# Kernel tuning notes

Measured on AMD Instinct MI355X. Metric: run time of the kernel, lower is better.

## Reference

```python
import jax, jax.numpy as jnp
import numpy as np

NEG = -1e6

def setup_inputs() -> dict:
    key = jax.random.key(0)
    ks = jax.random.split(key, 7)
    B, Q, K, H, Dv = 16, 64, 1024, 256, 256
    return {
        "queries": jax.random.normal(ks[0], (B, Q, H), jnp.float32),
        "keys": jax.random.normal(ks[1], (B, K, H), jnp.float32),
        "values": jax.random.normal(ks[2], (B, K, Dv), jnp.float32),
        "valid_lens": jax.random.randint(ks[3], (B,), 1, K + 1),
        "Wq": jax.random.normal(ks[4], (H, H), jnp.float32) / np.sqrt(H),
        "Wk": jax.random.normal(ks[5], (H, H), jnp.float32) / np.sqrt(H),
        "wv": jax.random.normal(ks[6], (H,), jnp.float32) / np.sqrt(H),
    }

def reference(queries, keys, values, valid_lens, Wq, Wk, wv):
    # projections: [B,Q,H], [B,K,H]
    q = jnp.einsum("bqd,hd->bqh", queries, Wq)
    k = jnp.einsum("bkd,hd->bkh", keys, Wk)
    # broadcast add + tanh: [B,Q,K,H]
    features = jnp.tanh(q[:, :, None, :] + k[:, None, :, :])
    # score reduction over hidden: [B,Q,K]
    scores = jnp.einsum("bqkh,h->bqk", features, wv)
    # masked softmax over the key axis (1D valid_lens per batch)
    K = keys.shape[1]
    mask = jnp.arange(K)[None, None, :] < valid_lens[:, None, None]  # [B,1,K]
    scores = jnp.where(mask, scores, NEG)
    attn = jax.nn.softmax(scores, axis=-1)
    # weighted sum over values: [B,Q,Dv]
    return jnp.einsum("bqk,bkv->bqv", attn, values)
```

## Files before the change

kernel.cpp:

```cpp
#include <hip/hip_runtime.h>

#define LOG2E 1.4426950408889634f
#define TANH_SCALE 2.8853900817779268f
#define NEG_BIG -1e30f

typedef __attribute__((ext_vector_type(8))) short bf16x8;
typedef __attribute__((ext_vector_type(4))) float f32x4;

static __device__ __forceinline__ short f2bf(float f) {
    unsigned u = __builtin_bit_cast(unsigned, f);
    u += 0x7fffu + ((u >> 16) & 1u);
    return (short)(u >> 16);
}

__global__ __launch_bounds__(256) void proj_mfma(const float* __restrict__ queries,
                                                 const float* __restrict__ keys,
                                                 const float* __restrict__ Wq,
                                                 const float* __restrict__ Wk,
                                                 float* __restrict__ qp,
                                                 float* __restrict__ kp) {
    const int mtile = blockIdx.x;
    const float* A; const float* W; float* dst; int m0;
    if (mtile < 16) { A = queries; W = Wq; dst = qp; m0 = mtile * 64; }
    else            { A = keys;    W = Wk; dst = kp; m0 = (mtile - 16) * 64; }

    const int tid  = threadIdx.x;
    const int w    = tid >> 6;
    const int lane = tid & 63;
    const int wm   = w >> 1, wn = w & 1;
    const int row_base = m0 + wm * 32;
    const int col_base = blockIdx.y * 128 + wn * 64;
    const int r  = lane & 15;
    const int kq = lane >> 4;

    f32x4 acc[2][4] = {};

    #pragma unroll
    for (int ks = 0; ks < 8; ++ks) {
        const int k0 = ks * 32 + kq * 8;
        bf16x8 a[2], bb[4];
        #pragma unroll
        for (int mi = 0; mi < 2; ++mi) {
            const float* p = &A[(row_base + mi * 16 + r) * 256 + k0];
            float4 f0 = *reinterpret_cast<const float4*>(p);
            float4 f1 = *reinterpret_cast<const float4*>(p + 4);
            a[mi] = (bf16x8){f2bf(f0.x), f2bf(f0.y), f2bf(f0.z), f2bf(f0.w),
                             f2bf(f1.x), f2bf(f1.y), f2bf(f1.z), f2bf(f1.w)};
        }
        #pragma unroll
        for (int nj = 0; nj < 4; ++nj) {
            const float* p = &W[(col_base + nj * 16 + r) * 256 + k0];
            float4 f0 = *reinterpret_cast<const float4*>(p);
            float4 f1 = *reinterpret_cast<const float4*>(p + 4);
            bb[nj] = (bf16x8){f2bf(f0.x), f2bf(f0.y), f2bf(f0.z), f2bf(f0.w),
                              f2bf(f1.x), f2bf(f1.y), f2bf(f1.z), f2bf(f1.w)};
        }
        #pragma unroll
        for (int mi = 0; mi < 2; ++mi)
            #pragma unroll
            for (int nj = 0; nj < 4; ++nj)
                acc[mi][nj] = __builtin_amdgcn_mfma_f32_16x16x32_bf16(a[mi], bb[nj], acc[mi][nj], 0, 0, 0);
    }

    #pragma unroll
    for (int mi = 0; mi < 2; ++mi)
        #pragma unroll
        for (int nj = 0; nj < 4; ++nj)
            #pragma unroll
            for (int t = 0; t < 4; ++t)
                dst[(row_base + mi * 16 + kq * 4 + t) * 256 + col_base + nj * 16 + r] =
                    acc[mi][nj][t] * TANH_SCALE;
}

__global__ __launch_bounds__(256) void attn_kernel(const float* __restrict__ qp,
                                                   const float* __restrict__ kp,
                                                   const float* __restrict__ values,
                                                   const int* __restrict__ valid_lens,
                                                   const float* __restrict__ wv,
                                                   float* __restrict__ part_acc,
                                                   float* __restrict__ part_m,
                                                   float* __restrict__ part_l) {
    __shared__ float4 kp_t[64 * 32];
    __shared__ float4 qp_f4[4 * 64];
    __shared__ float4 wv2_f4[64];
    __shared__ float  p_lds[4][64];

    const int tid  = threadIdx.x;
    const int w    = tid >> 6;
    const int lane = tid & 63;
    const int qt = blockIdx.x, b = blockIdx.y, seg = blockIdx.z;
    const int q0 = qt << 2;
    const int q  = q0 + w;
    const int vl = valid_lens[b];
    const int kstart = seg << 8;
    const int pidx = (b * 64 + q) * 4 + seg;

    if (kstart >= vl) {
        f32x4 z = {0.f, 0.f, 0.f, 0.f};
        *reinterpret_cast<f32x4*>(&part_acc[pidx * 256 + lane * 4]) = z;
        if (lane == 0) { part_m[pidx] = NEG_BIG; part_l[pidx] = 0.0f; }
        return;
    }

    if (tid < 64) {
        float4 t = *reinterpret_cast<const float4*>(&wv[tid << 2]);
        float4 s2;
        s2.x = -2.0f * t.x; s2.y = -2.0f * t.y; s2.z = -2.0f * t.z; s2.w = -2.0f * t.w;
        wv2_f4[tid] = s2;
    }
    qp_f4[(w << 6) + lane] =
        *reinterpret_cast<const float4*>(&qp[(b * 64 + q) * 256 + (lane << 2)]);

    const int kend = min(kstart + 256, vl);
    const int nchunks = (kend - kstart + 63) >> 6;

    float m = -INFINITY, l = 0.0f;
    float acc0 = 0.f, acc1 = 0.f, acc2 = 0.f, acc3 = 0.f;

    for (int c = 0; c < nchunks; ++c) {
        const int ck = kstart + (c << 6);
        float s0 = 0.f, s1 = 0.f, s2 = 0.f, s3 = 0.f;

        #pragma unroll
        for (int half = 0; half < 2; ++half) {
            __syncthreads();
            {
                const float4* src = reinterpret_cast<const float4*>(&kp[(b * 1024 + ck) * 256]) + half * 32;
                #pragma unroll
                for (int i = 0; i < 8; ++i) {
                    int f   = tid + 256 * i;
                    int row = f >> 5;
                    int col = f & 31;
                    kp_t[(row << 5) + (col ^ (row & 7))] = src[row * 64 + col];
                }
            }
            __syncthreads();

            const int krow = lane << 5;
            const int ksw  = lane & 7;
            const int hq   = half << 5;
            #pragma unroll 8
            for (int jh = 0; jh < 32; ++jh) {
                float4 kv  = kp_t[krow + (jh ^ ksw)];
                float4 qv  = qp_f4[(w << 6) + hq + jh];
                float4 wvv = wv2_f4[hq + jh];
                s0 += wvv.x * __builtin_amdgcn_rcpf(__builtin_amdgcn_exp2f(kv.x + qv.x) + 1.0f);
                s1 += wvv.y * __builtin_amdgcn_rcpf(__builtin_amdgcn_exp2f(kv.y + qv.y) + 1.0f);
                s2 += wvv.z * __builtin_amdgcn_rcpf(__builtin_amdgcn_exp2f(kv.z + qv.z) + 1.0f);
                s3 += wvv.w * __builtin_amdgcn_rcpf(__builtin_amdgcn_exp2f(kv.w + qv.w) + 1.0f);
            }
        }
        float s = (s0 + s1) + (s2 + s3);
        if (ck + lane >= vl) s = NEG_BIG;

        float mc = s;
        #pragma unroll
        for (int o = 32; o > 0; o >>= 1) mc = fmaxf(mc, __shfl_xor(mc, o));
        float m_new = fmaxf(m, mc);
        float rr = __builtin_amdgcn_exp2f((m - m_new) * LOG2E);
        float p  = __builtin_amdgcn_exp2f((s - m_new) * LOG2E);
        float lc = p;
        #pragma unroll
        for (int o = 32; o > 0; o >>= 1) lc += __shfl_xor(lc, o);
        l = l * rr + lc;
        m = m_new;
        acc0 *= rr; acc1 *= rr; acc2 *= rr; acc3 *= rr;
        p_lds[w][lane] = p;

        const int nv = min(64, kend - ck);
        const float* vsrc = &values[(b * 1024 + ck) * 256 + (lane << 2)];
        if (nv == 64) {
            #pragma unroll 8
            for (int j = 0; j < 64; ++j) {
                float pj = p_lds[w][j];
                float4 v = *reinterpret_cast<const float4*>(&vsrc[j * 256]);
                acc0 += pj * v.x; acc1 += pj * v.y; acc2 += pj * v.z; acc3 += pj * v.w;
            }
        } else {
            for (int j = 0; j < nv; ++j) {
                float pj = p_lds[w][j];
                float4 v = *reinterpret_cast<const float4*>(&vsrc[j * 256]);
                acc0 += pj * v.x; acc1 += pj * v.y; acc2 += pj * v.z; acc3 += pj * v.w;
            }
        }
    }

    if (lane == 0) { part_m[pidx] = m; part_l[pidx] = l; }
    f32x4 av = {acc0, acc1, acc2, acc3};
    *reinterpret_cast<f32x4*>(&part_acc[pidx * 256 + lane * 4]) = av;
}

__global__ __launch_bounds__(256) void combine_kernel(const float* __restrict__ part_acc,
                                                      const float* __restrict__ part_m,
                                                      const float* __restrict__ part_l,
                                                      float* __restrict__ out) {
    const int tid  = threadIdx.x;
    const int w    = tid >> 6;
    const int lane = tid & 63;
    const int b  = blockIdx.x >> 4;
    const int qt = blockIdx.x & 15;
    const int q  = (qt << 2) + w;
    const int base = (b * 64 + q) * 4;

    float m0 = part_m[base + 0], m1 = part_m[base + 1];
    float m2 = part_m[base + 2], m3 = part_m[base + 3];
    float M = fmaxf(fmaxf(m0, m1), fmaxf(m2, m3));
    float w0 = __builtin_amdgcn_exp2f((m0 - M) * LOG2E);
    float w1 = __builtin_amdgcn_exp2f((m1 - M) * LOG2E);
    float w2 = __builtin_amdgcn_exp2f((m2 - M) * LOG2E);
    float w3 = __builtin_amdgcn_exp2f((m3 - M) * LOG2E);
    float L = w0 * part_l[base + 0] + w1 * part_l[base + 1]
            + w2 * part_l[base + 2] + w3 * part_l[base + 3];

    const float* a0 = &part_acc[(base + 0) * 256 + (lane << 2)];
    float4 v0 = *reinterpret_cast<const float4*>(a0);
    float4 v1 = *reinterpret_cast<const float4*>(a0 + 256);
    float4 v2 = *reinterpret_cast<const float4*>(a0 + 512);
    float4 v3 = *reinterpret_cast<const float4*>(a0 + 768);
    float invL = 1.0f / L;
    float4 o;
    o.x = (w0 * v0.x + w1 * v1.x + w2 * v2.x + w3 * v3.x) * invL;
    o.y = (w0 * v0.y + w1 * v1.y + w2 * v2.y + w3 * v3.y) * invL;
    o.z = (w0 * v0.z + w1 * v1.z + w2 * v2.z + w3 * v3.z) * invL;
    o.w = (w0 * v0.w + w1 * v1.w + w2 * v2.w + w3 * v3.w) * invL;
    *reinterpret_cast<float4*>(&out[(b * 64 + q) * 256 + (lane << 2)]) = o;
}

extern "C" void kernel_launch(void* const* d_in, const int* in_sizes, int n_in,
                              void* d_out, int out_size, void* d_ws, size_t ws_size,
                              hipStream_t stream) {
    const float* queries    = (const float*)d_in[0];
    const float* keys       = (const float*)d_in[1];
    const float* values     = (const float*)d_in[2];
    const int*   valid_lens = (const int*)d_in[3];
    const float* Wq         = (const float*)d_in[4];
    const float* Wk         = (const float*)d_in[5];
    const float* wv         = (const float*)d_in[6];
    float* out = (float*)d_out;

    float* qp       = (float*)d_ws;
    float* kp       = qp + 262144;
    float* part_acc = kp + 4194304;
    float* part_m   = part_acc + 1048576;
    float* part_l   = part_m + 4096;

    proj_mfma<<<dim3(272, 2), 256, 0, stream>>>(queries, keys, Wq, Wk, qp, kp);
    attn_kernel<<<dim3(16, 16, 4), 256, 0, stream>>>(qp, kp, values, valid_lens, wv,
                                                     part_acc, part_m, part_l);
    combine_kernel<<<dim3(256), 256, 0, stream>>>(part_acc, part_m, part_l, out);
}
```

Measured before the change: 181.8 us.

## Factor tanh exponentials into projections, two queries per wave, finer key split

The projection kernel now stores exp2(scale*q) and exp2(scale*k), so the inner attention loop computes the tanh term as rcp(eq*ek+1) and needs no per-element exp. Each wave now handles two queries, reusing every key element loaded from LDS and every value row for both. The key axis is split into 8 segments of 128 instead of 4 of 256, and the combine kernel merges 8 partials. The projection GEMM also stages bf16 tiles through swizzled LDS instead of loading fragments directly from global memory. Precomputed exponentials can overflow for large projections, and the extra partials add workspace traffic.

```diff
diff --git a/kernel.cpp b/kernel.cpp
--- a/kernel.cpp
+++ b/kernel.cpp
@@ -17,49 +17,78 @@
                                                  const float* __restrict__ keys,
                                                  const float* __restrict__ Wq,
                                                  const float* __restrict__ Wk,
-                                                 float* __restrict__ qp,
-                                                 float* __restrict__ kp) {
+                                                 float* __restrict__ eq,
+                                                 float* __restrict__ ek) {
+    __shared__ char As[64 * 128];
+    __shared__ char Bs[128 * 128];
+
     const int mtile = blockIdx.x;
     const float* A; const float* W; float* dst; int m0;
-    if (mtile < 16) { A = queries; W = Wq; dst = qp; m0 = mtile * 64; }
-    else            { A = keys;    W = Wk; dst = kp; m0 = (mtile - 16) * 64; }
-
-    const int tid  = threadIdx.x;
-    const int w    = tid >> 6;
-    const int lane = tid & 63;
-    const int wm   = w >> 1, wn = w & 1;
-    const int row_base = m0 + wm * 32;
-    const int col_base = blockIdx.y * 128 + wn * 64;
-    const int r  = lane & 15;
-    const int kq = lane >> 4;
+    if (mtile < 16) { A = queries; W = Wq; dst = eq; m0 = mtile << 6; }
+    else            { A = keys;    W = Wk; dst = ek; m0 = (mtile - 16) << 6; }
+
+    const int tid = threadIdx.x;
+    const int w = tid >> 6, lane = tid & 63;
+    const int wm = w >> 1, wn = w & 1;
+    const int n0 = blockIdx.y << 7;
+    const int r = lane & 15, kq = lane >> 4;
 
     f32x4 acc[2][4] = {};
 
-    #pragma unroll
-    for (int ks = 0; ks < 8; ++ks) {
-        const int k0 = ks * 32 + kq * 8;
-        bf16x8 a[2], bb[4];
-        #pragma unroll
-        for (int mi = 0; mi < 2; ++mi) {
-            const float* p = &A[(row_base + mi * 16 + r) * 256 + k0];
-            float4 f0 = *reinterpret_cast<const float4*>(p);
-            float4 f1 = *reinterpret_cast<const float4*>(p + 4);
-            a[mi] = (bf16x8){f2bf(f0.x), f2bf(f0.y), f2bf(f0.z), f2bf(f0.w),
+    const int ra = tid >> 2, sa = tid & 3;
+    const int rb = tid >> 1, hb = tid & 1;
+
+    for (int ks = 0; ks < 4; ++ks) {
+        const int k0 = ks << 6;
+        __syncthreads();
+        {
+            const float* srcA = &A[(m0 + ra) * 256 + k0 + (sa << 4)];
+            #pragma unroll
+            for (int g = 0; g < 2; ++g) {
+                float4 f0 = *reinterpret_cast<const float4*>(srcA + (g << 3));
+                float4 f1 = *reinterpret_cast<const float4*>(srcA + (g << 3) + 4);
+                bf16x8 pk = {f2bf(f0.x), f2bf(f0.y), f2bf(f0.z), f2bf(f0.w),
                              f2bf(f1.x), f2bf(f1.y), f2bf(f1.z), f2bf(f1.w)};
-        }
-        #pragma unroll
-        for (int nj = 0; nj < 4; ++nj) {
-            const float* p = &W[(col_base + nj * 16 + r) * 256 + k0];
-            float4 f0 = *reinterpret_cast<const float4*>(p);
-            float4 f1 = *reinterpret_cast<const float4*>(p + 4);
-            bb[nj] = (bf16x8){f2bf(f0.x), f2bf(f0.y), f2bf(f0.z), f2bf(f0.w),
-                              f2bf(f1.x), f2bf(f1.y), f2bf(f1.z), f2bf(f1.w)};
-        }
-        #pragma unroll
-        for (int mi = 0; mi < 2; ++mi)
-            #pragma unroll
-            for (int nj = 0; nj < 4; ++nj)
-                acc[mi][nj] = __builtin_amdgcn_mfma_f32_16x16x32_bf16(a[mi], bb[nj], acc[mi][nj], 0, 0, 0);
+                int byt = (ra << 7) + (((sa << 5) + (g << 4)) ^ ((ra & 7) << 4));
+                *reinterpret_cast<bf16x8*>(As + byt) = pk;
+            }
+            const float* srcB = &W[(n0 + rb) * 256 + k0 + (hb << 5)];
+            #pragma unroll
+            for (int g = 0; g < 4; ++g) {
+                float4 f0 = *reinterpret_cast<const float4*>(srcB + (g << 3));
+                float4 f1 = *reinterpret_cast<const float4*>(srcB + (g << 3) + 4);
+                bf16x8 pk = {f2bf(f0.x), f2bf(f0.y), f2bf(f0.z), f2bf(f0.w),
+                             f2bf(f1.x), f2bf(f1.y), f2bf(f1.z), f2bf(f1.w)};
+                int byt = (rb << 7) + (((hb << 6) + (g << 4)) ^ ((rb & 7) << 4));
+                *reinterpret_cast<bf16x8*>(Bs + byt) = pk;
+            }
+        }
+        __syncthreads();
+
+        bf16x8 af[2][2], bfr[4][2];
+        #pragma unroll
+        for (int kf = 0; kf < 2; ++kf) {
+            #pragma unroll
+            for (int mi = 0; mi < 2; ++mi) {
+                int row = (wm << 5) + (mi << 4) + r;
+                int byt = (row << 7) + (((kf << 6) + (kq << 4)) ^ ((row & 7) << 4));
+                af[mi][kf] = *reinterpret_cast<const bf16x8*>(As + byt);
+            }
+            #pragma unroll
+            for (int nj = 0; nj < 4; ++nj) {
+                int row = (wn << 6) + (nj << 4) + r;
+                int byt = (row << 7) + (((kf << 6) + (kq << 4)) ^ ((row & 7) << 4));
+                bfr[nj][kf] = *reinterpret_cast<const bf16x8*>(Bs + byt);
+            }
+        }
+        #pragma unroll
+        for (int kf = 0; kf < 2; ++kf)
+            #pragma unroll
+            for (int mi = 0; mi < 2; ++mi)
+                #pragma unroll
+                for (int nj = 0; nj < 4; ++nj)
+                    acc[mi][nj] = __builtin_amdgcn_mfma_f32_16x16x32_bf16(
+                        af[mi][kf], bfr[nj][kf], acc[mi][nj], 0, 0, 0);
     }
 
     #pragma unroll
@@ -67,163 +96,179 @@
         #pragma unroll
         for (int nj = 0; nj < 4; ++nj)
             #pragma unroll
-            for (int t = 0; t < 4; ++t)
-                dst[(row_base + mi * 16 + kq * 4 + t) * 256 + col_base + nj * 16 + r] =
-                    acc[mi][nj][t] * TANH_SCALE;
-}
-
-__global__ __launch_bounds__(256) void attn_kernel(const float* __restrict__ qp,
-                                                   const float* __restrict__ kp,
+            for (int t = 0; t < 4; ++t) {
+                int row = m0 + (wm << 5) + (mi << 4) + (kq << 2) + t;
+                int col = n0 + (wn << 6) + (nj << 4) + r;
+                dst[row * 256 + col] = __builtin_amdgcn_exp2f(TANH_SCALE * acc[mi][nj][t]);
+            }
+}
+
+__global__ __launch_bounds__(256) void attn_kernel(const float* __restrict__ eq,
+                                                   const float* __restrict__ ek,
                                                    const float* __restrict__ values,
                                                    const int* __restrict__ valid_lens,
                                                    const float* __restrict__ wv,
                                                    float* __restrict__ part_acc,
                                                    float* __restrict__ part_m,
                                                    float* __restrict__ part_l) {
-    __shared__ float4 kp_t[64 * 32];
-    __shared__ float4 qp_f4[4 * 64];
-    __shared__ float4 wv2_f4[64];
-    __shared__ float  p_lds[4][64];
-
-    const int tid  = threadIdx.x;
-    const int w    = tid >> 6;
-    const int lane = tid & 63;
+    __shared__ float4 ek_lds[64 * 32];
+    __shared__ float p_lds[8][64];
+
+    const int tid = threadIdx.x;
+    const int w = tid >> 6, lane = tid & 63;
     const int qt = blockIdx.x, b = blockIdx.y, seg = blockIdx.z;
-    const int q0 = qt << 2;
-    const int q  = q0 + w;
+    const int q0 = (qt << 3) + (w << 1);
     const int vl = valid_lens[b];
-    const int kstart = seg << 8;
-    const int pidx = (b * 64 + q) * 4 + seg;
+    const int kstart = seg << 7;
+    const int pidx0 = (((b << 6) + q0) << 3) + seg;
 
     if (kstart >= vl) {
         f32x4 z = {0.f, 0.f, 0.f, 0.f};
-        *reinterpret_cast<f32x4*>(&part_acc[pidx * 256 + lane * 4]) = z;
-        if (lane == 0) { part_m[pidx] = NEG_BIG; part_l[pidx] = 0.0f; }
+        *reinterpret_cast<f32x4*>(&part_acc[(size_t)pidx0 * 256 + (lane << 2)]) = z;
+        *reinterpret_cast<f32x4*>(&part_acc[(size_t)(pidx0 + 8) * 256 + (lane << 2)]) = z;
+        if (lane == 0) {
+            part_m[pidx0] = NEG_BIG;     part_l[pidx0] = 0.f;
+            part_m[pidx0 + 8] = NEG_BIG; part_l[pidx0 + 8] = 0.f;
+        }
         return;
     }
 
-    if (tid < 64) {
-        float4 t = *reinterpret_cast<const float4*>(&wv[tid << 2]);
-        float4 s2;
-        s2.x = -2.0f * t.x; s2.y = -2.0f * t.y; s2.z = -2.0f * t.z; s2.w = -2.0f * t.w;
-        wv2_f4[tid] = s2;
-    }
-    qp_f4[(w << 6) + lane] =
-        *reinterpret_cast<const float4*>(&qp[(b * 64 + q) * 256 + (lane << 2)]);
-
-    const int kend = min(kstart + 256, vl);
+    const float4* eq0 = reinterpret_cast<const float4*>(&eq[((b << 6) + q0) * 256]);
+    const float4* eq1 = reinterpret_cast<const float4*>(&eq[((b << 6) + q0 + 1) * 256]);
+    const float4* wv4 = reinterpret_cast<const float4*>(wv);
+
+    const int kend = min(kstart + 128, vl);
     const int nchunks = (kend - kstart + 63) >> 6;
 
-    float m = -INFINITY, l = 0.0f;
-    float acc0 = 0.f, acc1 = 0.f, acc2 = 0.f, acc3 = 0.f;
+    float mA = -INFINITY, lA = 0.f, mB = -INFINITY, lB = 0.f;
+    f32x4 accA = {0.f, 0.f, 0.f, 0.f}, accB = {0.f, 0.f, 0.f, 0.f};
+
+    const int krow = lane << 5;
+    const int ksw = lane & 7;
 
     for (int c = 0; c < nchunks; ++c) {
         const int ck = kstart + (c << 6);
-        float s0 = 0.f, s1 = 0.f, s2 = 0.f, s3 = 0.f;
+        float s0 = 0.f, s1 = 0.f;
 
         #pragma unroll
         for (int half = 0; half < 2; ++half) {
             __syncthreads();
             {
-                const float4* src = reinterpret_cast<const float4*>(&kp[(b * 1024 + ck) * 256]) + half * 32;
+                const float4* src =
+                    reinterpret_cast<const float4*>(&ek[(size_t)(b * 1024 + ck) * 256]) + (half << 5);
                 #pragma unroll
                 for (int i = 0; i < 8; ++i) {
-                    int f   = tid + 256 * i;
-                    int row = f >> 5;
-                    int col = f & 31;
-                    kp_t[(row << 5) + (col ^ (row & 7))] = src[row * 64 + col];
+                    int d = (i << 8) + tid;
+                    int row = d >> 5, col = d & 31;
+                    ek_lds[(row << 5) + (col ^ (row & 7))] = src[row * 64 + col];
                 }
             }
             __syncthreads();
 
-            const int krow = lane << 5;
-            const int ksw  = lane & 7;
-            const int hq   = half << 5;
+            const int hoff = half << 5;
             #pragma unroll 8
             for (int jh = 0; jh < 32; ++jh) {
-                float4 kv  = kp_t[krow + (jh ^ ksw)];
-                float4 qv  = qp_f4[(w << 6) + hq + jh];
-                float4 wvv = wv2_f4[hq + jh];
-                s0 += wvv.x * __builtin_amdgcn_rcpf(__builtin_amdgcn_exp2f(kv.x + qv.x) + 1.0f);
-                s1 += wvv.y * __builtin_amdgcn_rcpf(__builtin_amdgcn_exp2f(kv.y + qv.y) + 1.0f);
-                s2 += wvv.z * __builtin_amdgcn_rcpf(__builtin_amdgcn_exp2f(kv.z + qv.z) + 1.0f);
-                s3 += wvv.w * __builtin_amdgcn_rcpf(__builtin_amdgcn_exp2f(kv.w + qv.w) + 1.0f);
-            }
-        }
-        float s = (s0 + s1) + (s2 + s3);
-        if (ck + lane >= vl) s = NEG_BIG;
-
-        float mc = s;
-        #pragma unroll
-        for (int o = 32; o > 0; o >>= 1) mc = fmaxf(mc, __shfl_xor(mc, o));
-        float m_new = fmaxf(m, mc);
-        float rr = __builtin_amdgcn_exp2f((m - m_new) * LOG2E);
-        float p  = __builtin_amdgcn_exp2f((s - m_new) * LOG2E);
-        float lc = p;
-        #pragma unroll
-        for (int o = 32; o > 0; o >>= 1) lc += __shfl_xor(lc, o);
-        l = l * rr + lc;
-        m = m_new;
-        acc0 *= rr; acc1 *= rr; acc2 *= rr; acc3 *= rr;
-        p_lds[w][lane] = p;
+                float4 kv = ek_lds[krow + (jh ^ ksw)];
+                float4 qa = eq0[hoff + jh];
+                float4 qb = eq1[hoff + jh];
+                float4 wc = wv4[hoff + jh];
+                s0 += wc.x * __builtin_amdgcn_rcpf(fmaf(kv.x, qa.x, 1.0f));
+                s0 += wc.y * __builtin_amdgcn_rcpf(fmaf(kv.y, qa.y, 1.0f));
+                s0 += wc.z * __builtin_amdgcn_rcpf(fmaf(kv.z, qa.z, 1.0f));
+                s0 += wc.w * __builtin_amdgcn_rcpf(fmaf(kv.w, qa.w, 1.0f));
+                s1 += wc.x * __builtin_amdgcn_rcpf(fmaf(kv.x, qb.x, 1.0f));
+                s1 += wc.y * __builtin_amdgcn_rcpf(fmaf(kv.y, qb.y, 1.0f));
+                s1 += wc.z * __builtin_amdgcn_rcpf(fmaf(kv.z, qb.z, 1.0f));
+                s1 += wc.w * __builtin_amdgcn_rcpf(fmaf(kv.w, qb.w, 1.0f));
+            }
+        }
+        float sA = -2.0f * s0;
+        float sB = -2.0f * s1;
+        if (ck + lane >= vl) { sA = NEG_BIG; sB = NEG_BIG; }
+
+        float mcA = sA, mcB = sB;
+        #pragma unroll
+        for (int o = 32; o > 0; o >>= 1) {
+            mcA = fmaxf(mcA, __shfl_xor(mcA, o));
+            mcB = fmaxf(mcB, __shfl_xor(mcB, o));
+        }
+        float mnA = fmaxf(mA, mcA), mnB = fmaxf(mB, mcB);
+        float rA = __builtin_amdgcn_exp2f((mA - mnA) * LOG2E);
+        float rB = __builtin_amdgcn_exp2f((mB - mnB) * LOG2E);
+        float pA = __builtin_amdgcn_exp2f((sA - mnA) * LOG2E);
+        float pB = __builtin_amdgcn_exp2f((sB - mnB) * LOG2E);
+        float lcA = pA, lcB = pB;
+        #pragma unroll
+        for (int o = 32; o > 0; o >>= 1) {
+            lcA += __shfl_xor(lcA, o);
+            lcB += __shfl_xor(lcB, o);
+        }
+        lA = lA * rA + lcA; mA = mnA;
+        lB = lB * rB + lcB; mB = mnB;
+        accA *= rA; accB *= rB;
+        p_lds[(w << 1) + 0][lane] = pA;
+        p_lds[(w << 1) + 1][lane] = pB;
 
         const int nv = min(64, kend - ck);
-        const float* vsrc = &values[(b * 1024 + ck) * 256 + (lane << 2)];
+        const float* vsrc = &values[(size_t)(b * 1024 + ck) * 256 + (lane << 2)];
         if (nv == 64) {
             #pragma unroll 8
             for (int j = 0; j < 64; ++j) {
-                float pj = p_lds[w][j];
-                float4 v = *reinterpret_cast<const float4*>(&vsrc[j * 256]);
-                acc0 += pj * v.x; acc1 += pj * v.y; acc2 += pj * v.z; acc3 += pj * v.w;
+                float pa = p_lds[(w << 1)][j], pb = p_lds[(w << 1) + 1][j];
+                float4 v = *reinterpret_cast<const float4*>(vsrc + j * 256);
+                accA.x += pa * v.x; accA.y += pa * v.y; accA.z += pa * v.z; accA.w += pa * v.w;
+                accB.x += pb * v.x; accB.y += pb * v.y; accB.z += pb * v.z; accB.w += pb * v.w;
             }
         } else {
             for (int j = 0; j < nv; ++j) {
-                float pj = p_lds[w][j];
-                float4 v = *reinterpret_cast<const float4*>(&vsrc[j * 256]);
-                acc0 += pj * v.x; acc1 += pj * v.y; acc2 += pj * v.z; acc3 += pj * v.w;
-            }
-        }
-    }
-
-    if (lane == 0) { part_m[pidx] = m; part_l[pidx] = l; }
-    f32x4 av = {acc0, acc1, acc2, acc3};
-    *reinterpret_cast<f32x4*>(&part_acc[pidx * 256 + lane * 4]) = av;
+                float pa = p_lds[(w << 1)][j], pb = p_lds[(w << 1) + 1][j];
+                float4 v = *reinterpret_cast<const float4*>(vsrc + j * 256);
+                accA.x += pa * v.x; accA.y += pa * v.y; accA.z += pa * v.z; accA.w += pa * v.w;
+                accB.x += pb * v.x; accB.y += pb * v.y; accB.z += pb * v.z; accB.w += pb * v.w;
+            }
+        }
+    }
+
+    if (lane == 0) {
+        part_m[pidx0] = mA;     part_l[pidx0] = lA;
+        part_m[pidx0 + 8] = mB; part_l[pidx0 + 8] = lB;
+    }
+    *reinterpret_cast<f32x4*>(&part_acc[(size_t)pidx0 * 256 + (lane << 2)]) = accA;
+    *reinterpret_cast<f32x4*>(&part_acc[(size_t)(pidx0 + 8) * 256 + (lane << 2)]) = accB;
 }
 
 __global__ __launch_bounds__(256) void combine_kernel(const float* __restrict__ part_acc,
                                                       const float* __restrict__ part_m,
                                                       const float* __restrict__ part_l,
                                                       float* __restrict__ out) {
-    const int tid  = threadIdx.x;
-    const int w    = tid >> 6;
-    const int lane = tid & 63;
-    const int b  = blockIdx.x >> 4;
-    const int qt = blockIdx.x & 15;
-    const int q  = (qt << 2) + w;
-    const int base = (b * 64 + q) * 4;
-
-    float m0 = part_m[base + 0], m1 = part_m[base + 1];
-    float m2 = part_m[base + 2], m3 = part_m[base + 3];
-    float M = fmaxf(fmaxf(m0, m1), fmaxf(m2, m3));
-    float w0 = __builtin_amdgcn_exp2f((m0 - M) * LOG2E);
-    float w1 = __builtin_amdgcn_exp2f((m1 - M) * LOG2E);
-    float w2 = __builtin_amdgcn_exp2f((m2 - M) * LOG2E);
-    float w3 = __builtin_amdgcn_exp2f((m3 - M) * LOG2E);
-    float L = w0 * part_l[base + 0] + w1 * part_l[base + 1]
-            + w2 * part_l[base + 2] + w3 * part_l[base + 3];
-
-    const float* a0 = &part_acc[(base + 0) * 256 + (lane << 2)];
-    float4 v0 = *reinterpret_cast<const float4*>(a0);
-    float4 v1 = *reinterpret_cast<const float4*>(a0 + 256);
-    float4 v2 = *reinterpret_cast<const float4*>(a0 + 512);
-    float4 v3 = *reinterpret_cast<const float4*>(a0 + 768);
+    const int tid = threadIdx.x;
+    const int w = tid >> 6, lane = tid & 63;
+    const int b = blockIdx.x >> 4, qt = blockIdx.x & 15;
+    const int q = (qt << 2) + w;
+    const int base = (((b << 6) + q) << 3);
+
+    float mm[8], ll[8];
+    #pragma unroll
+    for (int i = 0; i < 8; ++i) { mm[i] = part_m[base + i]; ll[i] = part_l[base + i]; }
+    float M = mm[0];
+    #pragma unroll
+    for (int i = 1; i < 8; ++i) M = fmaxf(M, mm[i]);
+    float wt[8];
+    float L = 0.f;
+    #pragma unroll
+    for (int i = 0; i < 8; ++i) {
+        wt[i] = __builtin_amdgcn_exp2f((mm[i] - M) * LOG2E);
+        L += wt[i] * ll[i];
+    }
     float invL = 1.0f / L;
-    float4 o;
-    o.x = (w0 * v0.x + w1 * v1.x + w2 * v2.x + w3 * v3.x) * invL;
-    o.y = (w0 * v0.y + w1 * v1.y + w2 * v2.y + w3 * v3.y) * invL;
-    o.z = (w0 * v0.z + w1 * v1.z + w2 * v2.z + w3 * v3.z) * invL;
-    o.w = (w0 * v0.w + w1 * v1.w + w2 * v2.w + w3 * v3.w) * invL;
-    *reinterpret_cast<float4*>(&out[(b * 64 + q) * 256 + (lane << 2)]) = o;
+    float4 o = {0.f, 0.f, 0.f, 0.f};
+    #pragma unroll
+    for (int i = 0; i < 8; ++i) {
+        float4 v = *reinterpret_cast<const float4*>(&part_acc[(size_t)(base + i) * 256 + (lane << 2)]);
+        o.x += wt[i] * v.x; o.y += wt[i] * v.y; o.z += wt[i] * v.z; o.w += wt[i] * v.w;
+    }
+    o.x *= invL; o.y *= invL; o.z *= invL; o.w *= invL;
+    *reinterpret_cast<float4*>(&out[((b << 6) + q) * 256 + (lane << 2)]) = o;
 }
 
 extern "C" void kernel_launch(void* const* d_in, const int* in_sizes, int n_in,
@@ -238,14 +283,14 @@
     const float* wv         = (const float*)d_in[6];
     float* out = (float*)d_out;
 
-    float* qp       = (float*)d_ws;
-    float* kp       = qp + 262144;
-    float* part_acc = kp + 4194304;
-    float* part_m   = part_acc + 1048576;
-    float* part_l   = part_m + 4096;
-
-    proj_mfma<<<dim3(272, 2), 256, 0, stream>>>(queries, keys, Wq, Wk, qp, kp);
-    attn_kernel<<<dim3(16, 16, 4), 256, 0, stream>>>(qp, kp, values, valid_lens, wv,
-                                                     part_acc, part_m, part_l);
+    float* eqw      = (float*)d_ws;
+    float* ekw      = eqw + 262144;
+    float* part_acc = ekw + 4194304;
+    float* part_m   = part_acc + 2097152;
+    float* part_l   = part_m + 8192;
+
+    proj_mfma<<<dim3(272, 2), 256, 0, stream>>>(queries, keys, Wq, Wk, eqw, ekw);
+    attn_kernel<<<dim3(8, 16, 8), 256, 0, stream>>>(eqw, ekw, values, valid_lens, wv,
+                                                    part_acc, part_m, part_l);
     combine_kernel<<<dim3(256), 256, 0, stream>>>(part_acc, part_m, part_l, out);
 }
```

New measurement: 162.9 us. 10.4% less time.
